# Optimization experiments

Hardware: AMD Instinct MI355X
Metric: run time of the kernel (lower is better)

The kernel has to match this reference:

```python
import jax, jax.numpy as jnp
import numpy as np

D_MODEL = 1024
NUM_HEADS = 16
HEAD_DIM = D_MODEL // NUM_HEADS


def setup_inputs() -> dict:
    key = jax.random.key(0)
    ks = jax.random.split(key, 5)
    x = jax.random.normal(ks[0], (2, 2048, D_MODEL), dtype=jnp.float32)
    s = 1.0 / np.sqrt(D_MODEL)
    # nn.Linear weight is [out, in]; y = x @ W.T
    Wq = jax.random.normal(ks[1], (D_MODEL, D_MODEL), dtype=jnp.float32) * s
    Wk = jax.random.normal(ks[2], (D_MODEL, D_MODEL), dtype=jnp.float32) * s
    Wv = jax.random.normal(ks[3], (D_MODEL, D_MODEL), dtype=jnp.float32) * s
    Wo = jax.random.normal(ks[4], (D_MODEL, D_MODEL), dtype=jnp.float32) * s
    return {"x": x, "Wq": Wq, "Wk": Wk, "Wv": Wv, "Wo": Wo}


def reference(x, Wq, Wk, Wv, Wo):
    b, s, d = x.shape
    h, hd = NUM_HEADS, HEAD_DIM
    # projections (Linear: x @ W.T), reshape to [b, h, s, hd]
    def proj(W):
        return (x @ W.T).reshape(b, s, h, hd).transpose(0, 2, 1, 3)
    Q, K, V = proj(Wq), proj(Wk), proj(Wv)
    # NOTE: original scales by 1/sqrt(d_model), not 1/sqrt(head_dim)
    scores = jnp.einsum('bhqd,bhkd->bhqk', Q, K) / jnp.sqrt(jnp.float32(d))
    attn = jax.nn.softmax(scores, axis=-1)
    ctx = jnp.einsum('bhqk,bhkd->bhqd', attn, V)
    ctx = ctx.transpose(0, 2, 1, 3).reshape(b, s, d)
    return ctx @ Wo.T
```

## Files before the change

kernel.cpp:

```cpp
#include <hip/hip_runtime.h>
#include <cstddef>
#include <cstdint>

#define SEQ 2048
#define DM 1024
#define NH 16
#define HD 64

typedef _Float16 f16;
typedef __attribute__((ext_vector_type(8))) _Float16 f16x8;
typedef __attribute__((ext_vector_type(4))) _Float16 f16x4;
typedef __attribute__((ext_vector_type(2))) _Float16 f16x2;
typedef __attribute__((ext_vector_type(4))) float f32x4;

__global__ __launch_bounds__(256) void cast_all(const float* __restrict__ x,
                                                const float* __restrict__ Wq,
                                                const float* __restrict__ Wk,
                                                const float* __restrict__ Wv,
                                                const float* __restrict__ Wo,
                                                f16* __restrict__ dst) {
  const int i = blockIdx.x * 256 + threadIdx.x;
  const float* src;
  int off;
  if (i < 1048576) {
    src = x; off = i;
  } else {
    const int j = i - 1048576;
    const int wsel = j >> 18;
    src = (wsel == 0) ? Wq : (wsel == 1) ? Wk : (wsel == 2) ? Wv : Wo;
    off = j & 262143;
  }
  const float4 v = ((const float4*)src)[off];
  f16x4 o = {(f16)v.x, (f16)v.y, (f16)v.z, (f16)v.w};
  ((f16x4*)dst)[i] = o;
}

__device__ __forceinline__ void gload16(const void* g, void* lds) {
  __builtin_amdgcn_global_load_lds((const __attribute__((address_space(1))) void*)g,
                                   (__attribute__((address_space(3))) void*)lds,
                                   16, 0, 0);
}

__device__ __forceinline__ void gemm_tile(const f16* __restrict__ A,
                                          const f16* __restrict__ B,
                                          f16* As, f16* Bs,
                                          int K, f32x4 acc[4][4]) {
  const int t = threadIdx.x;
  const int lane = t & 63;
  const int w = t >> 6;
  const int wm = (w & 1) << 6, wn = (w >> 1) << 6;
  const int srow = lane >> 3, sg = lane & 7;
  const int fr = lane & 15, q = lane >> 4;
  const int scol = (sg ^ srow) << 3;
  for (int k0 = 0; k0 < K; k0 += 64) {
    __syncthreads();
#pragma unroll
    for (int c = 0; c < 4; ++c) {
      const int row = (w << 5) + (c << 3) + srow;
      gload16(A + (size_t)row * K + k0 + scol, As + (w << 11) + (c << 9));
      gload16(B + (size_t)row * K + k0 + scol, Bs + (w << 11) + (c << 9));
    }
    __syncthreads();
    f16x8 af[4][2], bf[4][2];
#pragma unroll
    for (int i = 0; i < 4; ++i) {
      const int row = wm + (i << 4) + fr;
#pragma unroll
      for (int kh = 0; kh < 2; ++kh)
        af[i][kh] = *(const f16x8*)(As + row * 64 +
                                    ((((kh << 2) | q) ^ (row & 7)) << 3));
    }
#pragma unroll
    for (int j = 0; j < 4; ++j) {
      const int row = wn + (j << 4) + fr;
#pragma unroll
      for (int kh = 0; kh < 2; ++kh)
        bf[j][kh] = *(const f16x8*)(Bs + row * 64 +
                                    ((((kh << 2) | q) ^ (row & 7)) << 3));
    }
#pragma unroll
    for (int kh = 0; kh < 2; ++kh)
#pragma unroll
      for (int i = 0; i < 4; ++i)
#pragma unroll
        for (int j = 0; j < 4; ++j)
          acc[i][j] = __builtin_amdgcn_mfma_f32_16x16x32_f16(af[i][kh], bf[j][kh],
                                                             acc[i][j], 0, 0, 0);
  }
}

#define QSCALE 0.04508422003f
__global__ __launch_bounds__(256) void gemm_qkv(
    const f16* __restrict__ xb, const f16* __restrict__ Wqb,
    const f16* __restrict__ Wkb, const f16* __restrict__ Wvb,
    f16* __restrict__ Qb, f16* __restrict__ Kb, f16* __restrict__ Vtg) {
  __shared__ f16 smem[16384];
  f16* As = smem;
  f16* Bs = smem + 8192;
  const int which = blockIdx.x >> 3;
  const int bn = (blockIdx.x & 7) << 7;
  const int bm = blockIdx.y << 7;
  const f16* B = (which == 0) ? Wqb : (which == 1) ? Wkb : Wvb;
  f32x4 acc[4][4] = {};
  gemm_tile(xb + (size_t)bm * DM, B + (size_t)bn * DM, As, Bs, DM, acc);
  const int lane = threadIdx.x & 63, w = threadIdx.x >> 6;
  const int wm = (w & 1) << 6, wn = (w >> 1) << 6;
  const int col = lane & 15, q = lane >> 4;
  if (which < 2) {
    f16* C = (which == 0) ? Qb : Kb;
    const float sc = (which == 0) ? QSCALE : 1.0f;
#pragma unroll
    for (int i = 0; i < 4; ++i) {
      const int m = bm + wm + (i << 4) + (q << 2);
#pragma unroll
      for (int j = 0; j < 4; ++j) {
        const int n = bn + wn + (j << 4) + col;
#pragma unroll
        for (int r = 0; r < 4; ++r)
          C[(size_t)(m + r) * DM + n] = (f16)(acc[i][j][r] * sc);
      }
    }
  } else {
    __syncthreads();
#pragma unroll
    for (int i = 0; i < 4; ++i) {
      const int m0 = wm + (i << 4) + (q << 2);
      const int cm = m0 >> 3, sub = (m0 >> 2) & 1;
#pragma unroll
      for (int j = 0; j < 4; ++j) {
        const int nl = wn + (j << 4) + col;
        f16x4 o = {(f16)acc[i][j][0], (f16)acc[i][j][1],
                   (f16)acc[i][j][2], (f16)acc[i][j][3]};
        *(f16x4*)(smem + nl * 128 +
                  ((cm ^ (nl & 15) ^ ((nl >> 4) & 3)) << 3) + (sub << 2)) = o;
      }
    }
    __syncthreads();
    const int b = bm >> 11, sb = bm & 2047;
    const int d = threadIdx.x & 63;
#pragma unroll
    for (int pr = 0; pr < 8; ++pr) {
      const int idx0 = (threadIdx.x >> 6) + (pr << 3);
      const int hh = idx0 >> 5;
      const int s40 = idx0 & 31;
      const int s41 = s40 + 4;
      const int nl = (hh << 6) + d;
      f16x4 va, vb;
      {
        const int cm = s40 >> 1, sub = s40 & 1;
        va = *(const f16x4*)(smem + nl * 128 +
                             ((cm ^ (nl & 15) ^ ((nl >> 4) & 3)) << 3) + (sub << 2));
      }
      {
        const int cm = s41 >> 1, sub = s41 & 1;
        vb = *(const f16x4*)(smem + nl * 128 +
                             ((cm ^ (nl & 15) ^ ((nl >> 4) & 3)) << 3) + (sub << 2));
      }
      const int bh = (b << 4) + (bn >> 6) + hh;
      const int kt = (sb >> 6) + (s40 >> 4);
      const int kc2 = (s40 & 15) >> 3, qd = s40 & 3;
      const f16x8 vv = __builtin_shufflevector(va, vb, 0, 1, 2, 3, 4, 5, 6, 7);
      const size_t flat = ((size_t)bh << 17) + ((size_t)kt << 12) +
                          ((size_t)kc2 << 11) + ((size_t)qd << 9) + ((size_t)d << 3);
      *(f16x8*)(Vtg + flat) = vv;
    }
  }
}

__global__ __launch_bounds__(256) void gemm_out(const f16* __restrict__ Ab,
                                                const f16* __restrict__ Wob,
                                                float* __restrict__ out) {
  __shared__ f16 As[128 * 64];
  __shared__ f16 Bs[64 * 64];
  const int bn = blockIdx.x << 6, bm = blockIdx.y << 7;
  const int t = threadIdx.x, lane = t & 63, w = t >> 6;
  const int srow = lane >> 3, sg = lane & 7;
  const int fr = lane & 15, q = lane >> 4;
  const int scol = (sg ^ srow) << 3;
  const f16* A = Ab + (size_t)bm * DM;
  const f16* B = Wob + (size_t)bn * DM;
  const int wm = w << 5;
  f32x4 acc[2][4] = {};
  for (int k0 = 0; k0 < DM; k0 += 64) {
    __syncthreads();
#pragma unroll
    for (int c = 0; c < 4; ++c) {
      const int row = (w << 5) + (c << 3) + srow;
      gload16(A + (size_t)row * DM + k0 + scol, As + (w << 11) + (c << 9));
    }
#pragma unroll
    for (int c = 0; c < 2; ++c) {
      const int row = (w << 4) + (c << 3) + srow;
      gload16(B + (size_t)row * DM + k0 + scol, Bs + (w << 10) + (c << 9));
    }
    __syncthreads();
    f16x8 af[2][2], bf[4][2];
#pragma unroll
    for (int i = 0; i < 2; ++i) {
      const int row = wm + (i << 4) + fr;
#pragma unroll
      for (int kh = 0; kh < 2; ++kh)
        af[i][kh] = *(const f16x8*)(As + row * 64 +
                                    ((((kh << 2) | q) ^ (row & 7)) << 3));
    }
#pragma unroll
    for (int j = 0; j < 4; ++j) {
      const int row = (j << 4) + fr;
#pragma unroll
      for (int kh = 0; kh < 2; ++kh)
        bf[j][kh] = *(const f16x8*)(Bs + row * 64 +
                                    ((((kh << 2) | q) ^ (row & 7)) << 3));
    }
#pragma unroll
    for (int kh = 0; kh < 2; ++kh)
#pragma unroll
      for (int i = 0; i < 2; ++i)
#pragma unroll
        for (int j = 0; j < 4; ++j)
          acc[i][j] = __builtin_amdgcn_mfma_f32_16x16x32_f16(af[i][kh], bf[j][kh],
                                                             acc[i][j], 0, 0, 0);
  }
  const int col = lane & 15;
#pragma unroll
  for (int i = 0; i < 2; ++i) {
    const int m = bm + wm + (i << 4) + (q << 2);
#pragma unroll
    for (int j = 0; j < 4; ++j) {
      const int n = bn + (j << 4) + col;
#pragma unroll
      for (int r = 0; r < 4; ++r)
        out[(size_t)(m + r) * DM + n] = acc[i][j][r];
    }
  }
}

__global__ __launch_bounds__(256, 2) void attn_mfma(const f16* __restrict__ Qb,
                                                    const f16* __restrict__ Kb,
                                                    const f16* __restrict__ Vtg,
                                                    f16* __restrict__ Ctx) {
  __shared__ f16 smem[16384];
  const int t = threadIdx.x, lane = t & 63, w = t >> 6;
  const int fr = lane & 15, quad = lane >> 4;
  const int i = blockIdx.x;
  const int j = i >> 3;
  const int bh = ((i & 7) << 2) + (j >> 4);
  const int qt16 = j & 15;
  const int b = bh >> 4, h = bh & 15;

  const size_t qrow0 = (size_t)b * SEQ + qt16 * 128 + w * 32;

  f16x8 Qf[2][2];
#pragma unroll
  for (int qt = 0; qt < 2; ++qt)
#pragma unroll
    for (int hf = 0; hf < 2; ++hf)
      Qf[qt][hf] = *(const f16x8*)(Qb + (qrow0 + qt * 16 + fr) * DM + h * HD +
                                   hf * 32 + (quad << 3));

  const int krow = lane >> 2;
  const int kkc = ((lane & 3) - (lane >> 3)) & 3;
  const f16* Kg = Kb + ((size_t)b * SEQ + 16 * w + krow) * DM + h * HD + (kkc << 3);
  const f16* Vg = Vtg + ((size_t)bh << 17) + (((w << 7) + lane) << 3);

  const int crd = ((fr >> 1) << 3) | ((fr & 1) << 2) | (((fr >> 1) + quad) & 3);

  f16* K0 = smem;
  f16* K1 = smem + 4096;
  f16* V0 = smem + 8192;
  f16* V1 = smem + 12288;

  auto stage = [&](int kt, f16* Kimg, f16* Vimg) {
#pragma unroll
    for (int hf = 0; hf < 2; ++hf)
      gload16(Kg + (size_t)kt * 64 * DM + hf * 32, Kimg + (hf << 11) + (w << 9));
#pragma unroll
    for (int c = 0; c < 2; ++c)
      gload16(Vg + kt * 4096 + (c << 9), Vimg + (w << 10) + (c << 9));
  };

  f32x4 acc[2][4] = {};
  float lacc[2] = {0.f, 0.f};
  f16x8 Kf[4][2], Vf[4][2], pf[2][2];

  auto frags = [&](const f16* KR, const f16* VR) {
#pragma unroll
    for (int mt = 0; mt < 4; ++mt)
#pragma unroll
      for (int hf = 0; hf < 2; ++hf)
        Kf[mt][hf] = *(const f16x8*)(KR + (crd << 3) + (hf << 11) + (mt << 9));
#pragma unroll
    for (int dt = 0; dt < 4; ++dt)
#pragma unroll
      for (int kc = 0; kc < 2; ++kc)
        Vf[dt][kc] = *(const f16x8*)(VR + (kc << 11) + (quad << 9) +
                                     (((dt << 4) | fr) << 3));
  };

  auto qkexp = [&]() {
    f32x4 z[2][4] = {};
#pragma unroll
    for (int hf = 0; hf < 2; ++hf)
#pragma unroll
      for (int qt = 0; qt < 2; ++qt)
#pragma unroll
        for (int mt = 0; mt < 4; ++mt)
          z[qt][mt] = __builtin_amdgcn_mfma_f32_16x16x32_f16(Kf[mt][hf], Qf[qt][hf],
                                                             z[qt][mt], 0, 0, 0);
#pragma unroll
    for (int qt = 0; qt < 2; ++qt) {
      f16x4 p4[4];
#pragma unroll
      for (int mt = 0; mt < 4; ++mt) {
        const float p0 = __builtin_amdgcn_exp2f(z[qt][mt][0]);
        const float p1 = __builtin_amdgcn_exp2f(z[qt][mt][1]);
        const float p2 = __builtin_amdgcn_exp2f(z[qt][mt][2]);
        const float p3 = __builtin_amdgcn_exp2f(z[qt][mt][3]);
        lacc[qt] += (p0 + p1) + (p2 + p3);
        const f16x2 lo = __builtin_bit_cast(f16x2, __builtin_amdgcn_cvt_pkrtz(p0, p1));
        const f16x2 hi = __builtin_bit_cast(f16x2, __builtin_amdgcn_cvt_pkrtz(p2, p3));
        f16x4 pv4; pv4.x = lo.x; pv4.y = lo.y; pv4.z = hi.x; pv4.w = hi.y;
        p4[mt] = pv4;
      }
      pf[qt][0] = __builtin_shufflevector(p4[0], p4[1], 0, 1, 2, 3, 4, 5, 6, 7);
      pf[qt][1] = __builtin_shufflevector(p4[2], p4[3], 0, 1, 2, 3, 4, 5, 6, 7);
    }
  };

  auto pv = [&]() {
#pragma unroll
    for (int kc = 0; kc < 2; ++kc)
#pragma unroll
      for (int dt = 0; dt < 4; ++dt)
#pragma unroll
        for (int qt = 0; qt < 2; ++qt)
          acc[qt][dt] = __builtin_amdgcn_mfma_f32_16x16x32_f16(Vf[dt][kc], pf[qt][kc],
                                                               acc[qt][dt], 0, 0, 0);
  };

  stage(0, K0, V0);

  __syncthreads();
  stage(1, K1, V1);
  frags(K0, V0);
  qkexp();

  for (int kt = 1; kt < 31; kt += 2) {
    __syncthreads();
    stage(kt + 1, K0, V0);
    pv();
    frags(K1, V1);
    qkexp();
    __syncthreads();
    stage(kt + 2, K1, V1);
    pv();
    frags(K0, V0);
    qkexp();
  }

  __syncthreads();
  pv();
  frags(K1, V1);
  qkexp();
  pv();

  float inv[2];
#pragma unroll
  for (int qt = 0; qt < 2; ++qt) {
    float l = lacc[qt];
    l += __shfl_xor(l, 16);
    l += __shfl_xor(l, 32);
    inv[qt] = __builtin_amdgcn_rcpf(l);
  }

  __syncthreads();
  f16* T = smem + (w << 11);
#pragma unroll
  for (int qt = 0; qt < 2; ++qt)
#pragma unroll
    for (int dt = 0; dt < 4; ++dt) {
      f16x4 o = {(f16)(acc[qt][dt][0] * inv[qt]), (f16)(acc[qt][dt][1] * inv[qt]),
                 (f16)(acc[qt][dt][2] * inv[qt]), (f16)(acc[qt][dt][3] * inv[qt])};
      *(f16x4*)(T + (qt * 16 + fr) * 64 + dt * 16 + (quad << 2)) = o;
    }
#pragma unroll
  for (int p = 0; p < 4; ++p) {
    const int ql = p * 8 + (lane >> 3);
    const f16x8 v = *(const f16x8*)(T + ql * 64 + ((lane & 7) << 3));
    *(f16x8*)(Ctx + (qrow0 + ql) * DM + h * HD + ((lane & 7) << 3)) = v;
  }
}

extern "C" void kernel_launch(void* const* d_in, const int* in_sizes, int n_in,
                              void* d_out, int out_size, void* d_ws, size_t ws_size,
                              hipStream_t stream) {
  const float* x  = (const float*)d_in[0];
  const float* Wq = (const float*)d_in[1];
  const float* Wk = (const float*)d_in[2];
  const float* Wv = (const float*)d_in[3];
  const float* Wo = (const float*)d_in[4];

  char* ws = (char*)d_ws;
  f16* xb  = (f16*)(ws);
  f16* Wb  = (f16*)(ws + (8u << 20));
  f16* Wqb = Wb;
  f16* Wkb = Wb + 1048576;
  f16* Wvb = Wb + 2097152;
  f16* Wob = Wb + 3145728;
  f16* Qb  = (f16*)(ws + (16u << 20));
  f16* Kb  = (f16*)(ws + (24u << 20));
  f16* Vtg = (f16*)(ws + (32u << 20));
  f16* Ctx = (f16*)(ws + (40u << 20));

  cast_all<<<8192, 256, 0, stream>>>(x, Wq, Wk, Wv, Wo, xb);

  gemm_qkv<<<dim3(24, 32), 256, 0, stream>>>(xb, Wqb, Wkb, Wvb, Qb, Kb, Vtg);
  attn_mfma<<<dim3(2 * NH * (SEQ / 128)), 256, 0, stream>>>(Qb, Kb, Vtg, Ctx);
  gemm_out<<<dim3(16, 32), 256, 0, stream>>>(Ctx, Wob, (float*)d_out);
}
```

Baseline: 183.6 us.

## Double-buffer GEMM LDS tiles with 32-wide K slices to overlap loads and MFMA

Both the QKV projection GEMM and the output projection GEMM now split each 64-wide K step into two 32-wide halves held in separate LDS buffers. The next half is prefetched with global_load_lds while the current half is fed to MFMA, replacing the old load-sync-compute-sync sequence with an overlapped ping-pong. The XOR swizzle is dropped, since the rows are now 32 halves wide, which may bring LDS bank conflicts back on fragment reads. Synchronization still occurs once per 32-wide K slice.

```diff
diff --git a/kernel.cpp b/kernel.cpp
--- a/kernel.cpp
+++ b/kernel.cpp
@@ -41,51 +41,47 @@
                                    16, 0, 0);
 }
 
-__device__ __forceinline__ void gemm_tile(const f16* __restrict__ A,
-                                          const f16* __restrict__ B,
-                                          f16* As, f16* Bs,
-                                          int K, f32x4 acc[4][4]) {
-  const int t = threadIdx.x;
-  const int lane = t & 63;
-  const int w = t >> 6;
+__device__ __forceinline__ void gemm_tile_db(const f16* __restrict__ A,
+                                             const f16* __restrict__ B,
+                                             f16* As0, f16* Bs0,
+                                             f16* As1, f16* Bs1,
+                                             int K, f32x4 acc[4][4]) {
+  const int t = threadIdx.x, lane = t & 63, w = t >> 6;
   const int wm = (w & 1) << 6, wn = (w >> 1) << 6;
-  const int srow = lane >> 3, sg = lane & 7;
+  const int srow = lane >> 2, scol = (lane & 3) << 3;
   const int fr = lane & 15, q = lane >> 4;
-  const int scol = (sg ^ srow) << 3;
+  auto stg = [&](int k0, f16* As, f16* Bs) {
+#pragma unroll
+    for (int c = 0; c < 2; ++c) {
+      const int chunk = (w << 1) + c;
+      const int row = (chunk << 4) + srow;
+      gload16(A + (size_t)row * K + k0 + scol, As + (chunk << 9));
+      gload16(B + (size_t)row * K + k0 + scol, Bs + (chunk << 9));
+    }
+  };
+  auto comp = [&](const f16* As, const f16* Bs) {
+    f16x8 af[4], bf[4];
+#pragma unroll
+    for (int i = 0; i < 4; ++i)
+      af[i] = *(const f16x8*)(As + (wm + (i << 4) + fr) * 32 + (q << 3));
+#pragma unroll
+    for (int j = 0; j < 4; ++j)
+      bf[j] = *(const f16x8*)(Bs + (wn + (j << 4) + fr) * 32 + (q << 3));
+#pragma unroll
+    for (int i = 0; i < 4; ++i)
+#pragma unroll
+      for (int j = 0; j < 4; ++j)
+        acc[i][j] = __builtin_amdgcn_mfma_f32_16x16x32_f16(af[i], bf[j],
+                                                           acc[i][j], 0, 0, 0);
+  };
+  stg(0, As0, Bs0);
   for (int k0 = 0; k0 < K; k0 += 64) {
     __syncthreads();
-#pragma unroll
-    for (int c = 0; c < 4; ++c) {
-      const int row = (w << 5) + (c << 3) + srow;
-      gload16(A + (size_t)row * K + k0 + scol, As + (w << 11) + (c << 9));
-      gload16(B + (size_t)row * K + k0 + scol, Bs + (w << 11) + (c << 9));
-    }
-    __syncthreads();
-    f16x8 af[4][2], bf[4][2];
-#pragma unroll
-    for (int i = 0; i < 4; ++i) {
-      const int row = wm + (i << 4) + fr;
-#pragma unroll
-      for (int kh = 0; kh < 2; ++kh)
-        af[i][kh] = *(const f16x8*)(As + row * 64 +
-                                    ((((kh << 2) | q) ^ (row & 7)) << 3));
-    }
-#pragma unroll
-    for (int j = 0; j < 4; ++j) {
-      const int row = wn + (j << 4) + fr;
-#pragma unroll
-      for (int kh = 0; kh < 2; ++kh)
-        bf[j][kh] = *(const f16x8*)(Bs + row * 64 +
-                                    ((((kh << 2) | q) ^ (row & 7)) << 3));
-    }
-#pragma unroll
-    for (int kh = 0; kh < 2; ++kh)
-#pragma unroll
-      for (int i = 0; i < 4; ++i)
-#pragma unroll
-        for (int j = 0; j < 4; ++j)
-          acc[i][j] = __builtin_amdgcn_mfma_f32_16x16x32_f16(af[i][kh], bf[j][kh],
-                                                             acc[i][j], 0, 0, 0);
+    stg(k0 + 32, As1, Bs1);
+    comp(As0, Bs0);
+    __syncthreads();
+    if (k0 + 64 < K) stg(k0 + 64, As0, Bs0);
+    comp(As1, Bs1);
   }
 }
 
@@ -95,14 +91,17 @@
     const f16* __restrict__ Wkb, const f16* __restrict__ Wvb,
     f16* __restrict__ Qb, f16* __restrict__ Kb, f16* __restrict__ Vtg) {
   __shared__ f16 smem[16384];
-  f16* As = smem;
-  f16* Bs = smem + 8192;
+  f16* As0 = smem;
+  f16* Bs0 = smem + 4096;
+  f16* As1 = smem + 8192;
+  f16* Bs1 = smem + 12288;
   const int which = blockIdx.x >> 3;
   const int bn = (blockIdx.x & 7) << 7;
   const int bm = blockIdx.y << 7;
   const f16* B = (which == 0) ? Wqb : (which == 1) ? Wkb : Wvb;
   f32x4 acc[4][4] = {};
-  gemm_tile(xb + (size_t)bm * DM, B + (size_t)bn * DM, As, Bs, DM, acc);
+  gemm_tile_db(xb + (size_t)bm * DM, B + (size_t)bn * DM, As0, Bs0, As1, Bs1,
+               DM, acc);
   const int lane = threadIdx.x & 63, w = threadIdx.x >> 6;
   const int wm = (w & 1) << 6, wn = (w >> 1) << 6;
   const int col = lane & 15, q = lane >> 4;
@@ -170,55 +169,54 @@
 __global__ __launch_bounds__(256) void gemm_out(const f16* __restrict__ Ab,
                                                 const f16* __restrict__ Wob,
                                                 float* __restrict__ out) {
-  __shared__ f16 As[128 * 64];
-  __shared__ f16 Bs[64 * 64];
+  __shared__ f16 smem[12288];
+  f16* As0 = smem;
+  f16* As1 = smem + 4096;
+  f16* Bs0 = smem + 8192;
+  f16* Bs1 = smem + 10240;
   const int bn = blockIdx.x << 6, bm = blockIdx.y << 7;
   const int t = threadIdx.x, lane = t & 63, w = t >> 6;
-  const int srow = lane >> 3, sg = lane & 7;
+  const int srow = lane >> 2, scol = (lane & 3) << 3;
   const int fr = lane & 15, q = lane >> 4;
-  const int scol = (sg ^ srow) << 3;
   const f16* A = Ab + (size_t)bm * DM;
   const f16* B = Wob + (size_t)bn * DM;
   const int wm = w << 5;
   f32x4 acc[2][4] = {};
+  auto stg = [&](int k0, f16* As, f16* Bs) {
+#pragma unroll
+    for (int c = 0; c < 2; ++c) {
+      const int chunk = (w << 1) + c;
+      const int row = (chunk << 4) + srow;
+      gload16(A + (size_t)row * DM + k0 + scol, As + (chunk << 9));
+    }
+    {
+      const int row = (w << 4) + srow;
+      gload16(B + (size_t)row * DM + k0 + scol, Bs + (w << 9));
+    }
+  };
+  auto comp = [&](const f16* As, const f16* Bs) {
+    f16x8 af[2], bf[4];
+#pragma unroll
+    for (int i = 0; i < 2; ++i)
+      af[i] = *(const f16x8*)(As + (wm + (i << 4) + fr) * 32 + (q << 3));
+#pragma unroll
+    for (int j = 0; j < 4; ++j)
+      bf[j] = *(const f16x8*)(Bs + ((j << 4) + fr) * 32 + (q << 3));
+#pragma unroll
+    for (int i = 0; i < 2; ++i)
+#pragma unroll
+      for (int j = 0; j < 4; ++j)
+        acc[i][j] = __builtin_amdgcn_mfma_f32_16x16x32_f16(af[i], bf[j],
+                                                           acc[i][j], 0, 0, 0);
+  };
+  stg(0, As0, Bs0);
   for (int k0 = 0; k0 < DM; k0 += 64) {
     __syncthreads();
-#pragma unroll
-    for (int c = 0; c < 4; ++c) {
-      const int row = (w << 5) + (c << 3) + srow;
-      gload16(A + (size_t)row * DM + k0 + scol, As + (w << 11) + (c << 9));
-    }
-#pragma unroll
-    for (int c = 0; c < 2; ++c) {
-      const int row = (w << 4) + (c << 3) + srow;
-      gload16(B + (size_t)row * DM + k0 + scol, Bs + (w << 10) + (c << 9));
-    }
-    __syncthreads();
-    f16x8 af[2][2], bf[4][2];
-#pragma unroll
-    for (int i = 0; i < 2; ++i) {
-      const int row = wm + (i << 4) + fr;
-#pragma unroll
-      for (int kh = 0; kh < 2; ++kh)
-        af[i][kh] = *(const f16x8*)(As + row * 64 +
-                                    ((((kh << 2) | q) ^ (row & 7)) << 3));
-    }
-#pragma unroll
-    for (int j = 0; j < 4; ++j) {
-      const int row = (j << 4) + fr;
-#pragma unroll
-      for (int kh = 0; kh < 2; ++kh)
-        bf[j][kh] = *(const f16x8*)(Bs + row * 64 +
-                                    ((((kh << 2) | q) ^ (row & 7)) << 3));
-    }
-#pragma unroll
-    for (int kh = 0; kh < 2; ++kh)
-#pragma unroll
-      for (int i = 0; i < 2; ++i)
-#pragma unroll
-        for (int j = 0; j < 4; ++j)
-          acc[i][j] = __builtin_amdgcn_mfma_f32_16x16x32_f16(af[i][kh], bf[j][kh],
-                                                             acc[i][j], 0, 0, 0);
+    stg(k0 + 32, As1, Bs1);
+    comp(As0, Bs0);
+    __syncthreads();
+    if (k0 + 64 < DM) stg(k0 + 64, As0, Bs0);
+    comp(As1, Bs1);
   }
   const int col = lane & 15;
 #pragma unroll
```

Result: no change. 182.2 us (-0.8%).

## Double-buffer LDS tiles in QKV and output projection GEMMs

Applied to the files above, without the earlier changes.

Both GEMM kernels now keep two LDS buffers and issue the async global-to-LDS loads for the next K-slice before running the MFMA work on the current slice. This lets memory loads overlap with matrix math instead of stalling at a barrier each iteration. The cost is double the shared memory per block: 64KB for the QKV GEMM and 48KB for the output GEMM. That may lower occupancy, and the kernels still rely on the barrier's wait-count to drain the prefetch.

```diff
diff --git a/kernel.cpp b/kernel.cpp
--- a/kernel.cpp
+++ b/kernel.cpp
@@ -41,26 +41,25 @@
                                    16, 0, 0);
 }
 
-__device__ __forceinline__ void gemm_tile(const f16* __restrict__ A,
-                                          const f16* __restrict__ B,
-                                          f16* As, f16* Bs,
-                                          int K, f32x4 acc[4][4]) {
-  const int t = threadIdx.x;
-  const int lane = t & 63;
-  const int w = t >> 6;
+__device__ __forceinline__ void gemm_tile_db(const f16* __restrict__ A,
+                                             const f16* __restrict__ B,
+                                             f16* As0, f16* Bs0,
+                                             f16* As1, f16* Bs1,
+                                             int K, f32x4 acc[4][4]) {
+  const int t = threadIdx.x, lane = t & 63, w = t >> 6;
   const int wm = (w & 1) << 6, wn = (w >> 1) << 6;
   const int srow = lane >> 3, sg = lane & 7;
   const int fr = lane & 15, q = lane >> 4;
   const int scol = (sg ^ srow) << 3;
-  for (int k0 = 0; k0 < K; k0 += 64) {
-    __syncthreads();
+  auto stg = [&](int k0, f16* As, f16* Bs) {
 #pragma unroll
     for (int c = 0; c < 4; ++c) {
       const int row = (w << 5) + (c << 3) + srow;
       gload16(A + (size_t)row * K + k0 + scol, As + (w << 11) + (c << 9));
       gload16(B + (size_t)row * K + k0 + scol, Bs + (w << 11) + (c << 9));
     }
-    __syncthreads();
+  };
+  auto comp = [&](const f16* As, const f16* Bs) {
     f16x8 af[4][2], bf[4][2];
 #pragma unroll
     for (int i = 0; i < 4; ++i) {
@@ -86,6 +85,15 @@
         for (int j = 0; j < 4; ++j)
           acc[i][j] = __builtin_amdgcn_mfma_f32_16x16x32_f16(af[i][kh], bf[j][kh],
                                                              acc[i][j], 0, 0, 0);
+  };
+  stg(0, As0, Bs0);
+  for (int k0 = 0; k0 < K; k0 += 128) {
+    __syncthreads();
+    stg(k0 + 64, As1, Bs1);
+    comp(As0, Bs0);
+    __syncthreads();
+    if (k0 + 128 < K) stg(k0 + 128, As0, Bs0);
+    comp(As1, Bs1);
   }
 }
 
@@ -94,15 +102,18 @@
     const f16* __restrict__ xb, const f16* __restrict__ Wqb,
     const f16* __restrict__ Wkb, const f16* __restrict__ Wvb,
     f16* __restrict__ Qb, f16* __restrict__ Kb, f16* __restrict__ Vtg) {
-  __shared__ f16 smem[16384];
-  f16* As = smem;
-  f16* Bs = smem + 8192;
+  __shared__ f16 smem[32768];
+  f16* As0 = smem;
+  f16* Bs0 = smem + 8192;
+  f16* As1 = smem + 16384;
+  f16* Bs1 = smem + 24576;
   const int which = blockIdx.x >> 3;
   const int bn = (blockIdx.x & 7) << 7;
   const int bm = blockIdx.y << 7;
   const f16* B = (which == 0) ? Wqb : (which == 1) ? Wkb : Wvb;
   f32x4 acc[4][4] = {};
-  gemm_tile(xb + (size_t)bm * DM, B + (size_t)bn * DM, As, Bs, DM, acc);
+  gemm_tile_db(xb + (size_t)bm * DM, B + (size_t)bn * DM, As0, Bs0, As1, Bs1,
+               DM, acc);
   const int lane = threadIdx.x & 63, w = threadIdx.x >> 6;
   const int wm = (w & 1) << 6, wn = (w >> 1) << 6;
   const int col = lane & 15, q = lane >> 4;
@@ -170,8 +181,11 @@
 __global__ __launch_bounds__(256) void gemm_out(const f16* __restrict__ Ab,
                                                 const f16* __restrict__ Wob,
                                                 float* __restrict__ out) {
-  __shared__ f16 As[128 * 64];
-  __shared__ f16 Bs[64 * 64];
+  __shared__ f16 smem[24576];
+  f16* As0 = smem;
+  f16* As1 = smem + 8192;
+  f16* Bs0 = smem + 16384;
+  f16* Bs1 = smem + 20480;
   const int bn = blockIdx.x << 6, bm = blockIdx.y << 7;
   const int t = threadIdx.x, lane = t & 63, w = t >> 6;
   const int srow = lane >> 3, sg = lane & 7;
@@ -181,8 +195,7 @@
   const f16* B = Wob + (size_t)bn * DM;
   const int wm = w << 5;
   f32x4 acc[2][4] = {};
-  for (int k0 = 0; k0 < DM; k0 += 64) {
-    __syncthreads();
+  auto stg = [&](int k0, f16* As, f16* Bs) {
 #pragma unroll
     for (int c = 0; c < 4; ++c) {
       const int row = (w << 5) + (c << 3) + srow;
@@ -193,7 +206,8 @@
       const int row = (w << 4) + (c << 3) + srow;
       gload16(B + (size_t)row * DM + k0 + scol, Bs + (w << 10) + (c << 9));
     }
-    __syncthreads();
+  };
+  auto comp = [&](const f16* As, const f16* Bs) {
     f16x8 af[2][2], bf[4][2];
 #pragma unroll
     for (int i = 0; i < 2; ++i) {
@@ -219,6 +233,15 @@
         for (int j = 0; j < 4; ++j)
           acc[i][j] = __builtin_amdgcn_mfma_f32_16x16x32_f16(af[i][kh], bf[j][kh],
                                                              acc[i][j], 0, 0, 0);
+  };
+  stg(0, As0, Bs0);
+  for (int k0 = 0; k0 < DM; k0 += 128) {
+    __syncthreads();
+    stg(k0 + 64, As1, Bs1);
+    comp(As0, Bs0);
+    __syncthreads();
+    if (k0 + 128 < DM) stg(k0 + 128, As0, Bs0);
+    comp(As1, Bs1);
   }
   const int col = lane & 15;
 #pragma unroll
```

Result: faster. 163.4 us (-11.0%).
